# Performance work log

Hardware: AMD Instinct MI355X
Metric: run time of the kernel (lower is better)

## Reference

```python
import jax, jax.numpy as jnp
import numpy as np

D_MODEL = 1024
NUM_HEADS = 16


def setup_inputs() -> dict:
    key = jax.random.key(0)
    ks = jax.random.split(key, 5)
    std = float(np.sqrt(2.0 / (D_MODEL + D_MODEL)))
    def w(k):
        # approximate trunc_normal init with clipped normal (init only; math of fwd unaffected)
        v = jax.random.truncated_normal(k, -3.0, 3.0, (D_MODEL, D_MODEL), jnp.float32) * std
        return v
    x = jax.random.normal(ks[0], (4, 2048, D_MODEL), jnp.float32)
    return {
        "x": x,
        "wq": w(ks[1]),
        "wk": w(ks[2]),
        "wv": w(ks[3]),
        "wo": w(ks[4]),
    }


def reference(x, wq, wk, wv, wo):
    b, s, d = x.shape
    h = NUM_HEADS
    dk = d // h
    # Linear: einsum('o i, ... i -> ... o')
    def proj(w):
        y = jnp.einsum('oi,bsi->bso', w, x)
        return y.reshape(b, s, h, dk).transpose(0, 2, 1, 3)  # b h s dk
    Q, K, V = proj(wq), proj(wk), proj(wv)
    scale = 1.0 / jnp.sqrt(jnp.asarray(dk, x.dtype))
    scores = jnp.einsum('bhqd,bhkd->bhqk', Q, K) * scale
    mask = jnp.tril(jnp.ones((s, s), dtype=bool))
    scores = jnp.where(mask, scores, -jnp.inf)
    attn = jax.nn.softmax(scores, axis=-1)
    out = jnp.einsum('bhqk,bhkd->bhqd', attn, V)
    out = out.transpose(0, 2, 1, 3).reshape(b, s, d)
    return jnp.einsum('oi,bsi->bso', wo, out)
```

## Files before the change

### kernel.cpp

```cpp
#include <hip/hip_runtime.h>
#include <hip/hip_bf16.h>


typedef __bf16 bf16x8 __attribute__((ext_vector_type(8)));
typedef __bf16 bf16x4 __attribute__((ext_vector_type(4)));
typedef float  f32x4  __attribute__((ext_vector_type(4)));
typedef float  f32x16 __attribute__((ext_vector_type(16)));
typedef unsigned int u32x4_t __attribute__((ext_vector_type(4)));

#define GLOBAL_AS __attribute__((address_space(1)))
#define LDS_AS    __attribute__((address_space(3)))

__device__ __forceinline__ void gload16(const void* g, void* l) {
    __builtin_amdgcn_global_load_lds((const GLOBAL_AS void*)g, (LDS_AS void*)l, 16, 0, 0);
}

__device__ __forceinline__ unsigned int cvtpk_bf16(float lo, float hi) {
    unsigned int r;
    asm("v_cvt_pk_bf16_f32 %0, %1, %2" : "=v"(r) : "v"(lo), "v"(hi));
    return r;
}

#define WAITVM6 asm volatile("s_waitcnt vmcnt(6)" ::: "memory")
#define WAITVM4 asm volatile("s_waitcnt vmcnt(4)" ::: "memory")
#define WAITVM0 asm volatile("s_waitcnt vmcnt(0)" ::: "memory")
#define SCHEDB  __builtin_amdgcn_sched_barrier(0)

__global__ __launch_bounds__(256) void cast_kernel(
    const float* __restrict__ x, const float* __restrict__ wq,
    const float* __restrict__ wk, const float* __restrict__ wv,
    const float* __restrict__ wo, __bf16* __restrict__ xb, __bf16* __restrict__ wb) {
    int bid = blockIdx.x;
    const float* src; __bf16* dst; int base;
    if (bid < 4096) {
        src = x; dst = xb; base = bid * 2048;
    } else {
        int r = bid - 4096; int wi = r >> 9;
        src = (wi == 0) ? wq : (wi == 1) ? wk : (wi == 2) ? wv : wo;
        dst = wb + wi * 1048576; base = (r & 511) * 2048;
    }
    int idx = base + threadIdx.x * 8;
    float4 a = *(const float4*)(src + idx);
    float4 b = *(const float4*)(src + idx + 4);
    bf16x8 o;
    o[0] = (__bf16)a.x; o[1] = (__bf16)a.y; o[2] = (__bf16)a.z; o[3] = (__bf16)a.w;
    o[4] = (__bf16)b.x; o[5] = (__bf16)b.y; o[6] = (__bf16)b.z; o[7] = (__bf16)b.w;
    *(bf16x8*)(dst + idx) = o;
}

__global__ __launch_bounds__(512, 2) void gemm_qkv_kernel(
    const __bf16* __restrict__ A, const __bf16* __restrict__ W,
    __bf16* __restrict__ Qb, __bf16* __restrict__ Kb, __bf16* __restrict__ Vt,
    float qscale) {
    __shared__ __align__(16) char lds[147456];
    const int t = threadIdx.x;
    const int wid = t >> 6, lane = t & 63;
    const int g = lane >> 4, m = lane & 15;
    const int wm = wid >> 2, wn = wid & 3;
    const int bid = (blockIdx.x & 7) * 96 + (blockIdx.x >> 3);
    const int mt = bid / 12, nt = bid % 12;
    const int m0 = mt * 128, n0 = nt * 256;
    const bool isV = (n0 >= 2048);

    const __bf16* sA[2]; int dA[2];
#pragma unroll
    for (int i = 0; i < 2; ++i) {
        const int ci = i * 512 + t;
        const int row = ci >> 3;
        const int k8 = (ci & 7) ^ (row & 7);
        sA[i] = A + (size_t)(m0 + row) * 1024 + k8 * 8;
        dA[i] = ci * 16;
    }
    const __bf16* sB[4]; int dB[4];
#pragma unroll
    for (int i = 0; i < 4; ++i) {
        const int ci = i * 512 + t;
        const int row = ci >> 3;
        const int k8 = (ci & 7) ^ (row & 7);
        sB[i] = W + (size_t)(n0 + row) * 1024 + k8 * 8;
        dB[i] = ci * 16;
    }
    auto stage = [&](int kt, char* buf) {
        gload16(sA[0] + kt * 64, buf + dA[0]);
        gload16(sA[1] + kt * 64, buf + dA[1]);
        gload16(sB[0] + kt * 64, buf + 16384 + dB[0]);
        gload16(sB[1] + kt * 64, buf + 16384 + dB[1]);
        gload16(sB[2] + kt * 64, buf + 16384 + dB[2]);
        gload16(sB[3] + kt * 64, buf + 16384 + dB[3]);
    };

    const int sw = (m & 7) << 4;
    const int offA = (wm * 64 + m) * 128 + ((g << 4) ^ sw);
    const int offB = (wn * 64 + m) * 128 + ((g << 4) ^ sw);

    stage(0, lds);
    stage(1, lds + 49152);
    WAITVM6;
    SCHEDB;
    __builtin_amdgcn_s_barrier();
    SCHEDB;

    f32x4 acc[4][4] = {};
    for (int kt = 0; kt < 16; ++kt) {
        char* cbuf = lds + (kt % 3) * 49152;
        if (kt < 14) stage(kt + 2, lds + ((kt + 2) % 3) * 49152);
        const char* bA = cbuf;
        const char* bB = cbuf + 16384;
        bf16x8 a0[4], b0[4], a1[4], b1[4];
#pragma unroll
        for (int i = 0; i < 4; ++i) {
            a0[i] = *(const bf16x8*)(bA + (offA + i * 2048));
            b0[i] = *(const bf16x8*)(bB + (offB + i * 2048));
            a1[i] = *(const bf16x8*)(bA + ((offA + i * 2048) ^ 64));
            b1[i] = *(const bf16x8*)(bB + ((offB + i * 2048) ^ 64));
        }
        __builtin_amdgcn_s_setprio(1);
        if (isV) {
#pragma unroll
            for (int mi = 0; mi < 4; ++mi)
#pragma unroll
                for (int ni = 0; ni < 4; ++ni)
                    acc[mi][ni] = __builtin_amdgcn_mfma_f32_16x16x32_bf16(a0[mi], b0[ni], acc[mi][ni], 0, 0, 0);
#pragma unroll
            for (int mi = 0; mi < 4; ++mi)
#pragma unroll
                for (int ni = 0; ni < 4; ++ni)
                    acc[mi][ni] = __builtin_amdgcn_mfma_f32_16x16x32_bf16(a1[mi], b1[ni], acc[mi][ni], 0, 0, 0);
        } else {
#pragma unroll
            for (int mi = 0; mi < 4; ++mi)
#pragma unroll
                for (int ni = 0; ni < 4; ++ni)
                    acc[mi][ni] = __builtin_amdgcn_mfma_f32_16x16x32_bf16(b0[ni], a0[mi], acc[mi][ni], 0, 0, 0);
#pragma unroll
            for (int mi = 0; mi < 4; ++mi)
#pragma unroll
                for (int ni = 0; ni < 4; ++ni)
                    acc[mi][ni] = __builtin_amdgcn_mfma_f32_16x16x32_bf16(b1[ni], a1[mi], acc[mi][ni], 0, 0, 0);
        }
        __builtin_amdgcn_s_setprio(0);
        if (kt < 14) { WAITVM6; }
        else if (kt == 14) { WAITVM0; }
        if (kt < 15) {
            SCHEDB;
            __builtin_amdgcn_s_barrier();
            SCHEDB;
        }
    }

    if (isV) {
        const int bb = m0 >> 11;
        const int sb = (m0 & 2047) + wm * 64 + 4 * g;
        const int hbase = ((n0 - 2048) >> 6) + wn;
#pragma unroll
        for (int mi = 0; mi < 4; ++mi)
#pragma unroll
            for (int ni = 0; ni < 4; ++ni) {
                const int d = ni * 16 + m;
                bf16x4 pk;
                pk[0] = (__bf16)(acc[mi][ni][0]); pk[1] = (__bf16)(acc[mi][ni][1]);
                pk[2] = (__bf16)(acc[mi][ni][2]); pk[3] = (__bf16)(acc[mi][ni][3]);
                *(bf16x4*)(Vt + ((size_t)(bb * 16 + hbase) * 64 + d) * 2048 + sb + mi * 16) = pk;
            }
    } else {
        __bf16* C = (n0 < 1024) ? Qb : Kb;
        const float sc = (n0 < 1024) ? qscale : 1.f;
        const int cb = (n0 & 1023) + wn * 64 + 4 * g;
        const int row = m0 + wm * 64 + m;
#pragma unroll
        for (int mi = 0; mi < 4; ++mi)
#pragma unroll
            for (int ni = 0; ni < 4; ++ni) {
                bf16x4 pk;
                pk[0] = (__bf16)(acc[mi][ni][0] * sc); pk[1] = (__bf16)(acc[mi][ni][1] * sc);
                pk[2] = (__bf16)(acc[mi][ni][2] * sc); pk[3] = (__bf16)(acc[mi][ni][3] * sc);
                *(bf16x4*)(C + (size_t)(row + mi * 16) * 1024 + cb + ni * 16) = pk;
            }
    }
}

__global__ __launch_bounds__(512, 2) void gemm_out_kernel(
    const __bf16* __restrict__ A, const __bf16* __restrict__ W, float* __restrict__ out) {
    __shared__ __align__(16) char lds[147456];
    const int t = threadIdx.x;
    const int wid = t >> 6, lane = t & 63;
    const int g = lane >> 4, m = lane & 15;
    const int wm = wid >> 2, wn = wid & 3;
    const int bid = (blockIdx.x & 7) * 32 + (blockIdx.x >> 3);
    const int mt = bid >> 2, nt = bid & 3;
    const int m0 = mt * 128, n0 = nt * 256;

    const __bf16* sA[2]; int dA[2];
#pragma unroll
    for (int i = 0; i < 2; ++i) {
        const int ci = i * 512 + t;
        const int row = ci >> 3;
        const int k8 = (ci & 7) ^ (row & 7);
        sA[i] = A + (size_t)(m0 + row) * 1024 + k8 * 8;
        dA[i] = ci * 16;
    }
    const __bf16* sB[4]; int dB[4];
#pragma unroll
    for (int i = 0; i < 4; ++i) {
        const int ci = i * 512 + t;
        const int row = ci >> 3;
        const int k8 = (ci & 7) ^ (row & 7);
        sB[i] = W + (size_t)(n0 + row) * 1024 + k8 * 8;
        dB[i] = ci * 16;
    }
    auto stage = [&](int kt, char* buf) {
        gload16(sA[0] + kt * 64, buf + dA[0]);
        gload16(sA[1] + kt * 64, buf + dA[1]);
        gload16(sB[0] + kt * 64, buf + 16384 + dB[0]);
        gload16(sB[1] + kt * 64, buf + 16384 + dB[1]);
        gload16(sB[2] + kt * 64, buf + 16384 + dB[2]);
        gload16(sB[3] + kt * 64, buf + 16384 + dB[3]);
    };

    const int sw = (m & 7) << 4;
    const int offA = (wm * 64 + m) * 128 + ((g << 4) ^ sw);
    const int offB = (wn * 64 + m) * 128 + ((g << 4) ^ sw);

    stage(0, lds);
    stage(1, lds + 49152);
    WAITVM6;
    SCHEDB;
    __builtin_amdgcn_s_barrier();
    SCHEDB;

    f32x4 acc[4][4] = {};
    for (int kt = 0; kt < 16; ++kt) {
        char* cbuf = lds + (kt % 3) * 49152;
        if (kt < 14) stage(kt + 2, lds + ((kt + 2) % 3) * 49152);
        const char* bA = cbuf;
        const char* bB = cbuf + 16384;
        bf16x8 a0[4], b0[4], a1[4], b1[4];
#pragma unroll
        for (int i = 0; i < 4; ++i) {
            a0[i] = *(const bf16x8*)(bA + (offA + i * 2048));
            b0[i] = *(const bf16x8*)(bB + (offB + i * 2048));
            a1[i] = *(const bf16x8*)(bA + ((offA + i * 2048) ^ 64));
            b1[i] = *(const bf16x8*)(bB + ((offB + i * 2048) ^ 64));
        }
        __builtin_amdgcn_s_setprio(1);
#pragma unroll
        for (int mi = 0; mi < 4; ++mi)
#pragma unroll
            for (int ni = 0; ni < 4; ++ni)
                acc[mi][ni] = __builtin_amdgcn_mfma_f32_16x16x32_bf16(b0[ni], a0[mi], acc[mi][ni], 0, 0, 0);
#pragma unroll
        for (int mi = 0; mi < 4; ++mi)
#pragma unroll
            for (int ni = 0; ni < 4; ++ni)
                acc[mi][ni] = __builtin_amdgcn_mfma_f32_16x16x32_bf16(b1[ni], a1[mi], acc[mi][ni], 0, 0, 0);
        __builtin_amdgcn_s_setprio(0);
        if (kt < 14) { WAITVM6; }
        else if (kt == 14) { WAITVM0; }
        if (kt < 15) {
            SCHEDB;
            __builtin_amdgcn_s_barrier();
            SCHEDB;
        }
    }

    const int row = m0 + wm * 64 + m;
    const int col = n0 + wn * 64 + 4 * g;
#pragma unroll
    for (int mi = 0; mi < 4; ++mi)
#pragma unroll
        for (int ni = 0; ni < 4; ++ni)
            *(f32x4*)(out + (size_t)(row + mi * 16) * 1024 + col + ni * 16) = acc[mi][ni];
}

__global__ __launch_bounds__(256) void attn_kernel(
    const __bf16* __restrict__ Qb, const __bf16* __restrict__ Kb,
    const __bf16* __restrict__ Vt, __bf16* __restrict__ Ob) {
    __shared__ __align__(16) char lds[32768];
    const int t = threadIdx.x;
    const int w = t >> 6, lane = t & 63;
    const int l31 = lane & 31, hi = lane >> 5;
    const int x = blockIdx.x;
    const int p = x >> 3;
    const int r = p >> 5, c = p & 31, j = c & 15;
    const int strip = (r & 1) ? (15 - j) : j;
    const int bh = (x & 7) | (((c >> 4) + 2 * r) << 3);
    const size_t sbase = (size_t)(bh >> 4) * 2048;
    const int hoff = (bh & 15) * 64;

    const int q0w = strip * 128 + w * 32;
    const int nt = 2 * (strip + 1);
    const int q = q0w + l31;

    const char* Kbase = (const char*)Kb + (sbase * 1024 + hoff) * 2;
    const char* Vbase = (const char*)Vt + (size_t)bh * 262144;
    const int srow = lane >> 3;
    const int scol = ((lane & 7) ^ srow) << 4;
    const int sw = (l31 & 7) << 4;
    int colx[4];
#pragma unroll
    for (int i = 0; i < 4; ++i) colx[i] = (32 * i + 16 * hi) ^ sw;

    auto stage = [&](int kv0, char* lK) {
        char* lV = lK + 8192;
#pragma unroll
        for (int i = 0; i < 2; ++i) {
            const int chunk = i * 4 + w;
            const int row = chunk * 8 + srow;
            gload16(Kbase + (size_t)(kv0 + row) * 2048 + scol, lK + chunk * 1024);
            gload16(Vbase + (size_t)row * 4096 + (size_t)kv0 * 2 + scol, lV + chunk * 1024);
        }
    };

    const __bf16* qrow = Qb + (sbase + q0w + l31) * 1024 + hoff + 8 * hi;
    bf16x8 qf[4];
#pragma unroll
    for (int cq = 0; cq < 4; ++cq) qf[cq] = *(const bf16x8*)(qrow + 16 * cq);

    f32x16 o0 = {}, o1 = {};
    float mrun = -__builtin_inff(), lrun = 0.f;

    stage(0, lds);

    for (int tt = 0; tt < nt; ++tt) {
        const int cur = tt & 1;
        char* lcur = lds + cur * 16384;
        __builtin_amdgcn_s_barrier();
        if (tt + 1 < nt) {
            stage((tt + 1) * 64, lds + (cur ^ 1) * 16384);
            WAITVM4;
        } else {
            WAITVM0;
        }
        __builtin_amdgcn_s_barrier();
        __builtin_amdgcn_sched_barrier(0);

        const int kv0 = tt * 64;
        const char* lK = lcur;
        const char* lV = lcur + 8192;

        f32x16 s0 = {}, s1 = {};
        __builtin_amdgcn_s_setprio(1);
#pragma unroll
        for (int cc = 0; cc < 4; ++cc) {
            bf16x8 k0 = *(const bf16x8*)(lK + l31 * 128 + colx[cc]);
            bf16x8 k1 = *(const bf16x8*)(lK + (l31 + 32) * 128 + colx[cc]);
            s0 = __builtin_amdgcn_mfma_f32_32x32x16_bf16(k0, qf[cc], s0, 0, 0, 0);
            s1 = __builtin_amdgcn_mfma_f32_32x32x16_bf16(k1, qf[cc], s1, 0, 0, 0);
        }
        __builtin_amdgcn_s_setprio(0);

        float pp[32];
#pragma unroll
        for (int rr = 0; rr < 16; ++rr) { pp[rr] = s0[rr]; pp[16 + rr] = s1[rr]; }
        if (kv0 + 63 > q0w) {
#pragma unroll
            for (int rr = 0; rr < 16; ++rr) {
                const int kvl = (rr & 3) + 8 * (rr >> 2) + 4 * hi;
                if (kv0 + kvl > q)      pp[rr]      = -__builtin_inff();
                if (kv0 + 32 + kvl > q) pp[16 + rr] = -__builtin_inff();
            }
        }
        float m8[8];
#pragma unroll
        for (int i = 0; i < 8; ++i)
            m8[i] = fmaxf(fmaxf(pp[4 * i], pp[4 * i + 1]), fmaxf(pp[4 * i + 2], pp[4 * i + 3]));
        float tmax = fmaxf(fmaxf(fmaxf(m8[0], m8[1]), fmaxf(m8[2], m8[3])),
                           fmaxf(fmaxf(m8[4], m8[5]), fmaxf(m8[6], m8[7])));
        const bool skip = __all(tmax <= mrun + 8.f);
        if (!skip) {
            float tq = fmaxf(tmax, __shfl_xor(tmax, 32));
            float mnew = fmaxf(mrun, tq);
            float al = __builtin_amdgcn_exp2f(mrun - mnew);
            lrun *= al;
#pragma unroll
            for (int rr = 0; rr < 16; ++rr) { o0[rr] *= al; o1[rr] *= al; }
            mrun = mnew;
        }
#pragma unroll
        for (int rr = 0; rr < 32; ++rr) pp[rr] = __builtin_amdgcn_exp2f(pp[rr] - mrun);
        float s8[8];
#pragma unroll
        for (int i = 0; i < 8; ++i)
            s8[i] = (pp[4 * i] + pp[4 * i + 1]) + (pp[4 * i + 2] + pp[4 * i + 3]);
        float rsum = ((s8[0] + s8[1]) + (s8[2] + s8[3])) + ((s8[4] + s8[5]) + (s8[6] + s8[7]));
        rsum += __shfl_xor(rsum, 32);
        lrun += rsum;

        __builtin_amdgcn_s_setprio(1);
#pragma unroll
        for (int cc = 0; cc < 4; ++cc) {
            const int pb = cc * 8;
            unsigned int A0 = cvtpk_bf16(pp[pb + 0], pp[pb + 1]);
            unsigned int A1 = cvtpk_bf16(pp[pb + 2], pp[pb + 3]);
            unsigned int B0 = cvtpk_bf16(pp[pb + 4], pp[pb + 5]);
            unsigned int B1 = cvtpk_bf16(pp[pb + 6], pp[pb + 7]);
            asm("v_permlane32_swap_b32 %0, %1" : "+v"(A0), "+v"(B0));
            asm("v_permlane32_swap_b32 %0, %1" : "+v"(A1), "+v"(B1));
            u32x4_t wvv; wvv[0] = A0; wvv[1] = A1; wvv[2] = B0; wvv[3] = B1;
            bf16x8 pa = __builtin_bit_cast(bf16x8, wvv);
            const int vcol = (32 * cc + 16 * hi) ^ sw;
            bf16x8 v0 = *(const bf16x8*)(lV + l31 * 128 + vcol);
            bf16x8 v1 = *(const bf16x8*)(lV + (l31 + 32) * 128 + vcol);
            o0 = __builtin_amdgcn_mfma_f32_32x32x16_bf16(v0, pa, o0, 0, 0, 0);
            o1 = __builtin_amdgcn_mfma_f32_32x32x16_bf16(v1, pa, o1, 0, 0, 0);
        }
        __builtin_amdgcn_s_setprio(0);
    }

    const float inv = 1.f / lrun;
    __bf16* orow = Ob + (sbase + q0w + l31) * 1024 + hoff;
#pragma unroll
    for (int rq = 0; rq < 4; ++rq) {
        bf16x4 e0, e1;
#pragma unroll
        for (int jj = 0; jj < 4; ++jj) {
            e0[jj] = (__bf16)(o0[rq * 4 + jj] * inv);
            e1[jj] = (__bf16)(o1[rq * 4 + jj] * inv);
        }
        *(bf16x4*)(orow + 4 * hi + 8 * rq) = e0;
        *(bf16x4*)(orow + 32 + 4 * hi + 8 * rq) = e1;
    }
}

extern "C" void kernel_launch(void* const* d_in, const int* in_sizes, int n_in,
                              void* d_out, int out_size, void* d_ws, size_t ws_size,
                              hipStream_t stream) {
    const float* x  = (const float*)d_in[0];
    const float* wq = (const float*)d_in[1];
    const float* wk = (const float*)d_in[2];
    const float* wv = (const float*)d_in[3];
    const float* wo = (const float*)d_in[4];

    char* ws = (char*)d_ws;
    __bf16* xb = (__bf16*)(ws);
    __bf16* wb = (__bf16*)(ws + 16777216);
    __bf16* Qb = (__bf16*)(ws + 25165824);
    __bf16* Kb = (__bf16*)(ws + 41943040);
    __bf16* Vt = (__bf16*)(ws + 58720256);
    __bf16* Ob = (__bf16*)(ws + 75497472);

    const float qscale = 0.18033688011112043f;

    cast_kernel<<<6144, 256, 0, stream>>>(x, wq, wk, wv, wo, xb, wb);
    gemm_qkv_kernel<<<768, 512, 0, stream>>>(xb, wb, Qb, Kb, Vt, qscale);
    attn_kernel<<<1024, 256, 0, stream>>>(Qb, Kb, Vt, Ob);
    gemm_out_kernel<<<256, 512, 0, stream>>>(Ob, wb + 3145728, (float*)d_out);
}
```

Baseline: 203.3 us.

## Pair complementary causal query tiles per attention block sharing streamed K/V

```diff
diff --git a/kernel.cpp b/kernel.cpp
--- a/kernel.cpp
+++ b/kernel.cpp
@@ -21,8 +21,8 @@
     return r;
 }
 
+#define WAITVM8 asm volatile("s_waitcnt vmcnt(8)" ::: "memory")
 #define WAITVM6 asm volatile("s_waitcnt vmcnt(6)" ::: "memory")
-#define WAITVM4 asm volatile("s_waitcnt vmcnt(4)" ::: "memory")
 #define WAITVM0 asm volatile("s_waitcnt vmcnt(0)" ::: "memory")
 #define SCHEDB  __builtin_amdgcn_sched_barrier(0)
 
@@ -272,24 +272,17 @@
             *(f32x4*)(out + (size_t)(row + mi * 16) * 1024 + col + ni * 16) = acc[mi][ni];
 }
 
-__global__ __launch_bounds__(256) void attn_kernel(
+__global__ __launch_bounds__(128, 2) void attn_kernel(
     const __bf16* __restrict__ Qb, const __bf16* __restrict__ Kb,
     const __bf16* __restrict__ Vt, __bf16* __restrict__ Ob) {
     __shared__ __align__(16) char lds[32768];
     const int t = threadIdx.x;
     const int w = t >> 6, lane = t & 63;
     const int l31 = lane & 31, hi = lane >> 5;
-    const int x = blockIdx.x;
-    const int p = x >> 3;
-    const int r = p >> 5, c = p & 31, j = c & 15;
-    const int strip = (r & 1) ? (15 - j) : j;
-    const int bh = (x & 7) | (((c >> 4) + 2 * r) << 3);
+    const int qb = (blockIdx.x >> 3) & 15;
+    const int bh = (blockIdx.x & 7) | ((blockIdx.x >> 7) << 3);
     const size_t sbase = (size_t)(bh >> 4) * 2048;
     const int hoff = (bh & 15) * 64;
-
-    const int q0w = strip * 128 + w * 32;
-    const int nt = 2 * (strip + 1);
-    const int q = q0w + l31;
 
     const char* Kbase = (const char*)Kb + (sbase * 1024 + hoff) * 2;
     const char* Vbase = (const char*)Vt + (size_t)bh * 262144;
@@ -303,61 +296,44 @@
     auto stage = [&](int kv0, char* lK) {
         char* lV = lK + 8192;
 #pragma unroll
-        for (int i = 0; i < 2; ++i) {
-            const int chunk = i * 4 + w;
+        for (int i = 0; i < 4; ++i) {
+            const int chunk = i * 2 + w;
             const int row = chunk * 8 + srow;
             gload16(Kbase + (size_t)(kv0 + row) * 2048 + scol, lK + chunk * 1024);
             gload16(Vbase + (size_t)row * 4096 + (size_t)kv0 * 2 + scol, lV + chunk * 1024);
         }
     };
 
-    const __bf16* qrow = Qb + (sbase + q0w + l31) * 1024 + hoff + 8 * hi;
-    bf16x8 qf[4];
-#pragma unroll
-    for (int cq = 0; cq < 4; ++cq) qf[cq] = *(const bf16x8*)(qrow + 16 * cq);
-
-    f32x16 o0 = {}, o1 = {};
-    float mrun = -__builtin_inff(), lrun = 0.f;
-
-    stage(0, lds);
-
-    for (int tt = 0; tt < nt; ++tt) {
-        const int cur = tt & 1;
-        char* lcur = lds + cur * 16384;
-        __builtin_amdgcn_s_barrier();
-        if (tt + 1 < nt) {
-            stage((tt + 1) * 64, lds + (cur ^ 1) * 16384);
-            WAITVM4;
-        } else {
-            WAITVM0;
-        }
-        __builtin_amdgcn_s_barrier();
-        __builtin_amdgcn_sched_barrier(0);
-
-        const int kv0 = tt * 64;
-        const char* lK = lcur;
-        const char* lV = lcur + 8192;
-
-        f32x16 s0 = {}, s1 = {};
-        __builtin_amdgcn_s_setprio(1);
-#pragma unroll
-        for (int cc = 0; cc < 4; ++cc) {
-            bf16x8 k0 = *(const bf16x8*)(lK + l31 * 128 + colx[cc]);
-            bf16x8 k1 = *(const bf16x8*)(lK + (l31 + 32) * 128 + colx[cc]);
-            s0 = __builtin_amdgcn_mfma_f32_32x32x16_bf16(k0, qf[cc], s0, 0, 0, 0);
-            s1 = __builtin_amdgcn_mfma_f32_32x32x16_bf16(k1, qf[cc], s1, 0, 0, 0);
-        }
-        __builtin_amdgcn_s_setprio(0);
-
+    const int q0A = qb * 64 + w * 32;
+    const int q0B = (31 - qb) * 64 + w * 32;
+    const int qA = q0A + l31, qB = q0B + l31;
+    const int nstream = 32 - qb;
+
+    const __bf16* qrowA = Qb + (sbase + q0A + l31) * 1024 + hoff + 8 * hi;
+    const __bf16* qrowB = Qb + (sbase + q0B + l31) * 1024 + hoff + 8 * hi;
+    bf16x8 qfA[4], qfB[4];
+#pragma unroll
+    for (int cq = 0; cq < 4; ++cq) {
+        qfA[cq] = *(const bf16x8*)(qrowA + 16 * cq);
+        qfB[cq] = *(const bf16x8*)(qrowB + 16 * cq);
+    }
+
+    f32x16 oA0 = {}, oA1 = {}, oB0 = {}, oB1 = {};
+    float mA = -__builtin_inff(), lA = 0.f;
+    float mB = -__builtin_inff(), lB = 0.f;
+
+    auto process = [&](const f32x16& s0r, const f32x16& s1r, int qq, bool diag,
+                       int kv0, float& mrun, float& lrun, f32x16& o0, f32x16& o1,
+                       const char* lV) {
         float pp[32];
 #pragma unroll
-        for (int rr = 0; rr < 16; ++rr) { pp[rr] = s0[rr]; pp[16 + rr] = s1[rr]; }
-        if (kv0 + 63 > q0w) {
+        for (int rr = 0; rr < 16; ++rr) { pp[rr] = s0r[rr]; pp[16 + rr] = s1r[rr]; }
+        if (diag) {
 #pragma unroll
             for (int rr = 0; rr < 16; ++rr) {
                 const int kvl = (rr & 3) + 8 * (rr >> 2) + 4 * hi;
-                if (kv0 + kvl > q)      pp[rr]      = -__builtin_inff();
-                if (kv0 + 32 + kvl > q) pp[16 + rr] = -__builtin_inff();
+                if (kv0 + kvl > qq)      pp[rr]      = -__builtin_inff();
+                if (kv0 + 32 + kvl > qq) pp[16 + rr] = -__builtin_inff();
             }
         }
         float m8[8];
@@ -405,20 +381,85 @@
             o1 = __builtin_amdgcn_mfma_f32_32x32x16_bf16(v1, pa, o1, 0, 0, 0);
         }
         __builtin_amdgcn_s_setprio(0);
-    }
-
-    const float inv = 1.f / lrun;
-    __bf16* orow = Ob + (sbase + q0w + l31) * 1024 + hoff;
-#pragma unroll
-    for (int rq = 0; rq < 4; ++rq) {
-        bf16x4 e0, e1;
-#pragma unroll
-        for (int jj = 0; jj < 4; ++jj) {
-            e0[jj] = (__bf16)(o0[rq * 4 + jj] * inv);
-            e1[jj] = (__bf16)(o1[rq * 4 + jj] * inv);
-        }
-        *(bf16x4*)(orow + 4 * hi + 8 * rq) = e0;
-        *(bf16x4*)(orow + 32 + 4 * hi + 8 * rq) = e1;
+    };
+
+    stage(0, lds);
+
+    for (int tt = 0; tt < nstream; ++tt) {
+        const int cur = tt & 1;
+        char* lcur = lds + cur * 16384;
+        __builtin_amdgcn_s_barrier();
+        if (tt + 1 < nstream) {
+            stage((tt + 1) * 64, lds + (cur ^ 1) * 16384);
+            WAITVM8;
+        } else {
+            WAITVM0;
+        }
+        __builtin_amdgcn_s_barrier();
+        __builtin_amdgcn_sched_barrier(0);
+
+        const int kv0 = tt * 64;
+        const char* lK = lcur;
+        const char* lV = lcur + 8192;
+        const bool dual = (tt <= qb);
+
+        f32x16 sA0 = {}, sA1 = {}, sB0 = {}, sB1 = {};
+        __builtin_amdgcn_s_setprio(1);
+        if (dual) {
+#pragma unroll
+            for (int cc = 0; cc < 4; ++cc) {
+                bf16x8 k0 = *(const bf16x8*)(lK + l31 * 128 + colx[cc]);
+                bf16x8 k1 = *(const bf16x8*)(lK + (l31 + 32) * 128 + colx[cc]);
+                sA0 = __builtin_amdgcn_mfma_f32_32x32x16_bf16(k0, qfA[cc], sA0, 0, 0, 0);
+                sA1 = __builtin_amdgcn_mfma_f32_32x32x16_bf16(k1, qfA[cc], sA1, 0, 0, 0);
+                sB0 = __builtin_amdgcn_mfma_f32_32x32x16_bf16(k0, qfB[cc], sB0, 0, 0, 0);
+                sB1 = __builtin_amdgcn_mfma_f32_32x32x16_bf16(k1, qfB[cc], sB1, 0, 0, 0);
+            }
+        } else {
+#pragma unroll
+            for (int cc = 0; cc < 4; ++cc) {
+                bf16x8 k0 = *(const bf16x8*)(lK + l31 * 128 + colx[cc]);
+                bf16x8 k1 = *(const bf16x8*)(lK + (l31 + 32) * 128 + colx[cc]);
+                sB0 = __builtin_amdgcn_mfma_f32_32x32x16_bf16(k0, qfB[cc], sB0, 0, 0, 0);
+                sB1 = __builtin_amdgcn_mfma_f32_32x32x16_bf16(k1, qfB[cc], sB1, 0, 0, 0);
+            }
+        }
+        __builtin_amdgcn_s_setprio(0);
+
+        if (dual)
+            process(sA0, sA1, qA, tt == qb, kv0, mA, lA, oA0, oA1, lV);
+        process(sB0, sB1, qB, tt == nstream - 1, kv0, mB, lB, oB0, oB1, lV);
+    }
+
+    {
+        const float inv = 1.f / lA;
+        __bf16* orow = Ob + (sbase + q0A + l31) * 1024 + hoff;
+#pragma unroll
+        for (int rq = 0; rq < 4; ++rq) {
+            bf16x4 e0, e1;
+#pragma unroll
+            for (int jj = 0; jj < 4; ++jj) {
+                e0[jj] = (__bf16)(oA0[rq * 4 + jj] * inv);
+                e1[jj] = (__bf16)(oA1[rq * 4 + jj] * inv);
+            }
+            *(bf16x4*)(orow + 4 * hi + 8 * rq) = e0;
+            *(bf16x4*)(orow + 32 + 4 * hi + 8 * rq) = e1;
+        }
+    }
+    {
+        const float inv = 1.f / lB;
+        __bf16* orow = Ob + (sbase + q0B + l31) * 1024 + hoff;
+#pragma unroll
+        for (int rq = 0; rq < 4; ++rq) {
+            bf16x4 e0, e1;
+#pragma unroll
+            for (int jj = 0; jj < 4; ++jj) {
+                e0[jj] = (__bf16)(oB0[rq * 4 + jj] * inv);
+                e1[jj] = (__bf16)(oB1[rq * 4 + jj] * inv);
+            }
+            *(bf16x4*)(orow + 4 * hi + 8 * rq) = e0;
+            *(bf16x4*)(orow + 32 + 4 * hi + 8 * rq) = e1;
+        }
     }
 }
 
@@ -443,6 +484,6 @@
 
     cast_kernel<<<6144, 256, 0, stream>>>(x, wq, wk, wv, wo, xb, wb);
     gemm_qkv_kernel<<<768, 512, 0, stream>>>(xb, wb, Qb, Kb, Vt, qscale);
-    attn_kernel<<<1024, 256, 0, stream>>>(Qb, Kb, Vt, Ob);
+    attn_kernel<<<1024, 128, 0, stream>>>(Qb, Kb, Vt, Ob);
     gemm_out_kernel<<<256, 512, 0, stream>>>(Ob, wb + 3145728, (float*)d_out);
 }
```

New measurement: 180.9 us. 1.12x faster.
